# Performance work log

Measured on AMD Instinct MI355X. Metric: run time of the kernel, lower is better.

The kernel has to match this reference:

```python
import jax, jax.numpy as jnp
import numpy as np
import math

B, CK, CV, O, T, H, W = 2, 64, 512, 2, 16, 30, 54


def setup_inputs() -> dict:
    key = jax.random.key(0)
    k1, k2, k3, k4, k5 = jax.random.split(key, 5)
    return {
        'query_key': jax.random.normal(k1, (B, CK, H, W), jnp.float32),
        'query_selection': jax.random.uniform(k2, (B, CK, H, W), jnp.float32),
        'memory_key': jax.random.normal(k3, (B, CK, T, H, W), jnp.float32),
        'memory_shrinkage': jax.random.uniform(k4, (B, 1, T, H, W), jnp.float32),
        'memory_value': jax.random.normal(k5, (B, O, CV, T, H, W), jnp.float32),
    }


def reference(query_key, query_selection, memory_key, memory_shrinkage, memory_value):
    b, ck, h, w = query_key.shape
    t = memory_key.shape[2]
    n = t * h * w          # memory bank size
    hw = h * w             # query size
    o, cv = memory_value.shape[1], memory_value.shape[2]

    mk = memory_key.reshape(b, ck, n)             # B CK N
    ms = memory_shrinkage.reshape(b, 1, n)        # B 1 N
    qk = query_key.reshape(b, ck, hw)             # B CK HW
    qe = query_selection.reshape(b, ck, hw)       # B CK HW

    # negative squared L2 distance, selection-weighted per channel:
    # -sum_c qe_c * (mk_c - qk_c)^2 = -a_sq + 2ab - b_sq
    a_sq = jnp.einsum('bcn,bcq->bnq', mk * mk, qe)          # B N HW
    two_ab = 2.0 * jnp.einsum('bcn,bcq->bnq', mk, qk * qe)  # B N HW
    b_sq = jnp.sum(qe * qk * qk, axis=1, keepdims=True)     # B 1 HW
    similarity = (-a_sq + two_ab - b_sq)
    # shrinkage scaling + 1/sqrt(CK)
    similarity = similarity * ms.reshape(b, n, 1) * (1.0 / math.sqrt(ck))

    # softmax over the memory axis N
    affinity = jax.nn.softmax(similarity, axis=1)           # B N HW

    # weighted readout
    mv = memory_value.reshape(b, o * cv, n)                 # B (O*CV) N
    mem = jnp.einsum('bvn,bnq->bvq', mv, affinity)          # B (O*CV) HW
    return mem.reshape(b, o, cv, h, w)
```

## Files before the change

### kernel.cpp

```cpp
#include <hip/hip_runtime.h>
#include <stdint.h>

#define CK 64
#define CKP 128
#define OCV 1024
#define NTOT 25920
#define HW 1620
#define HWP 1664
#define QT 128
#define VT 256
#define NC 64
#define NQT 13
#define NVT 4
#define NSPLIT 2
#define CHUNKS_TOTAL 405
#define CHUNK_SPLIT 203

typedef _Float16 f16x8 __attribute__((ext_vector_type(8)));
typedef _Float16 f16x4 __attribute__((ext_vector_type(4)));
typedef float f32x4 __attribute__((ext_vector_type(4)));

__device__ __forceinline__ void gload_lds16(const void* g, void* l) {
  __builtin_amdgcn_global_load_lds(
      (const __attribute__((address_space(1))) uint32_t*)g,
      (__attribute__((address_space(3))) uint32_t*)l, 16, 0, 0);
}

__global__ void k_prep_mv(const float* __restrict__ mv, _Float16* __restrict__ mvh) {
  int i = blockIdx.x * 256 + threadIdx.x;
  const float4* s = (const float4*)mv + (size_t)i * 2;
  float4 a = s[0], b = s[1];
  f16x8 o;
  o[0]=(_Float16)a.x; o[1]=(_Float16)a.y; o[2]=(_Float16)a.z; o[3]=(_Float16)a.w;
  o[4]=(_Float16)b.x; o[5]=(_Float16)b.y; o[6]=(_Float16)b.z; o[7]=(_Float16)b.w;
  *((f16x8*)mvh + i) = o;
}

__global__ void k_prep_mk(const float* __restrict__ mk, _Float16* __restrict__ mkp) {
  __shared__ _Float16 LT[64 * CKP];
  int b = blockIdx.y, n0 = blockIdx.x * 64;
  int c4 = threadIdx.x >> 6, nl = threadIdx.x & 63;
  for (int c = c4; c < 64; c += 4) {
    float v = mk[((size_t)(b * 64 + c)) * NTOT + n0 + nl];
    LT[nl * CKP + c]      = (_Float16)v;
    LT[nl * CKP + 64 + c] = (_Float16)(v * v);
  }
  __syncthreads();
  #pragma unroll
  for (int k = 0; k < 4; ++k) {
    int idx = threadIdx.x + 256 * k;
    int n = idx >> 4, c16 = idx & 15;
    *((uint4*)(mkp + ((size_t)b * NTOT + n0 + n) * CKP + c16 * 8)) =
        *((const uint4*)(&LT[n * CKP + c16 * 8]));
  }
}

__global__ void k_prep_q(const float* __restrict__ qk, const float* __restrict__ qe,
                         _Float16* __restrict__ qp, float* __restrict__ bsq) {
  __shared__ _Float16 LT[QT * CKP];
  int b = blockIdx.y, q0 = blockIdx.x * QT;
  int t = threadIdx.x;
  int q = q0 + t;
  bool valid = q < HW;
  float acc = 0.f;
  for (int c = 0; c < 64; ++c) {
    float a = valid ? qk[((size_t)(b * 64 + c)) * HW + q] : 0.f;
    float e = valid ? qe[((size_t)(b * 64 + c)) * HW + q] : 0.f;
    LT[t * CKP + c]      = (_Float16)(2.f * a * e);
    LT[t * CKP + 64 + c] = (_Float16)(-e);
    acc += e * a * a;
  }
  bsq[(size_t)b * HWP + q] = acc;
  __syncthreads();
  #pragma unroll
  for (int k = 0; k < 16; ++k) {
    int idx = t + 128 * k;
    int qq = idx >> 4, c16 = idx & 15;
    *((uint4*)(qp + ((size_t)b * HWP + q0 + qq) * CKP + c16 * 8)) =
        *((const uint4*)(&LT[qq * CKP + c16 * 8]));
  }
}

__launch_bounds__(512, 1)
__global__ void k_main(const _Float16* __restrict__ mvh, const _Float16* __restrict__ mkp,
                       const _Float16* __restrict__ qp, const float* __restrict__ bsq,
                       const float* __restrict__ ms,
                       float* __restrict__ pO, float* __restrict__ lpart) {
  const int qt = blockIdx.x, vt = blockIdx.y;
  const int b = blockIdx.z >> 1, nsp = blockIdx.z & 1;
  const int tid = threadIdx.x;
  const int w = tid >> 6, l = tid & 63;
  const int l15 = l & 15, g = l >> 4;

  __shared__ _Float16 Qs[QT * CKP];
  __shared__ _Float16 MKs[2][NC * CKP];
  __shared__ _Float16 MVs[2][VT * NC];
  __shared__ _Float16 Ps[QT * NC];
  __shared__ float bsqs[QT];
  __shared__ float lred[QT * 8];

  const int qw = w & 3, nh = w >> 2;
  const int wv = w & 3, wq = w >> 2;

  const int cBeg = nsp ? CHUNK_SPLIT : 0;
  const int cEnd = nsp ? CHUNKS_TOTAL : CHUNK_SPLIT;

  const char* mvb[4]; int dmv[4];
  #pragma unroll
  for (int k = 0; k < 4; ++k) {
    int idx = k * 512 + tid;
    int v = idx >> 3, s = idx & 7, j = s ^ (v & 7);
    mvb[k] = (const char*)(mvh + ((size_t)b * OCV + vt * VT + v) * NTOT + j * 8);
    dmv[k] = idx * 16;
  }
  const char* mkb[2]; int dmk[2];
  #pragma unroll
  for (int k = 0; k < 2; ++k) {
    int idx = k * 512 + tid;
    int n = idx >> 4, s = idx & 15, j = s ^ (n & 7);
    mkb[k] = (const char*)(mkp + ((size_t)b * NTOT + n) * CKP + j * 8);
    dmk[k] = idx * 16;
  }
  const float* msb = ms + (size_t)b * NTOT + nh * 32 + g * 4;

  {
    size_t omv = (size_t)cBeg * (NC * 2);
    size_t omk = (size_t)cBeg * (NC * CKP * 2);
    #pragma unroll
    for (int k = 0; k < 4; ++k) gload_lds16(mvb[k] + omv, (char*)MVs[0] + dmv[k]);
    #pragma unroll
    for (int k = 0; k < 2; ++k) gload_lds16(mkb[k] + omk, (char*)MKs[0] + dmk[k]);
  }
  #pragma unroll
  for (int k = 0; k < 4; ++k) {
    int s = tid + k * 512;
    int q = s >> 4, kb = s & 15;
    uint4 v = *((const uint4*)(qp + ((size_t)b * HWP + qt * QT + q) * CKP + kb * 8));
    *((uint4*)(&Qs[q * CKP + ((kb ^ (q & 7)) * 8)])) = v;
  }
  if (tid < QT) bsqs[tid] = bsq[(size_t)b * HWP + qt * QT + tid];
  __syncthreads();

  f32x4 acc[4][4];
  #pragma unroll
  for (int i = 0; i < 4; ++i)
    #pragma unroll
    for (int j = 0; j < 4; ++j) acc[i][j] = (f32x4)0.f;
  float lp0 = 0.f, lp1 = 0.f;

  int cur = 0;
  for (int ch = cBeg; ch < cEnd; ++ch) {
    const float4 msA = *(const float4*)(msb + (size_t)ch * NC);
    const float4 msB = *(const float4*)(msb + (size_t)ch * NC + 16);
    __builtin_amdgcn_sched_barrier(0);
    if (ch + 1 < cEnd) {
      size_t omv = (size_t)(ch + 1) * (NC * 2);
      size_t omk = (size_t)(ch + 1) * (NC * CKP * 2);
      char* dv = (char*)MVs[cur ^ 1];
      char* dk = (char*)MKs[cur ^ 1];
      #pragma unroll
      for (int k = 0; k < 4; ++k) gload_lds16(mvb[k] + omv, dv + dmv[k]);
      #pragma unroll
      for (int k = 0; k < 2; ++k) gload_lds16(mkb[k] + omk, dk + dmk[k]);
    }

    const _Float16* MKc = MKs[cur];
    f32x4 sacc[2][2];
    #pragma unroll
    for (int i = 0; i < 2; ++i)
      #pragma unroll
      for (int j = 0; j < 2; ++j) sacc[i][j] = (f32x4)0.f;
    #pragma unroll
    for (int ks = 0; ks < 4; ++ks) {
      f16x8 af[2], bf[2];
      #pragma unroll
      for (int i = 0; i < 2; ++i) {
        int n_loc = nh * 32 + i * 16 + l15;
        af[i] = *((const f16x8*)(&MKc[n_loc * CKP + (((ks * 4 + g) ^ (n_loc & 7)) * 8)]));
      }
      #pragma unroll
      for (int j = 0; j < 2; ++j) {
        int q_loc = qw * 32 + j * 16 + l15;
        bf[j] = *((const f16x8*)(&Qs[q_loc * CKP + (((ks * 4 + g) ^ (q_loc & 7)) * 8)]));
      }
      #pragma unroll
      for (int i = 0; i < 2; ++i)
        #pragma unroll
        for (int j = 0; j < 2; ++j)
          sacc[i][j] = __builtin_amdgcn_mfma_f32_16x16x32_f16(af[i], bf[j], sacc[i][j], 0, 0, 0);
    }

    const float K = 0.125f * 1.44269504f;
    #pragma unroll
    for (int i = 0; i < 2; ++i) {
      int nbase = nh * 32 + i * 16 + g * 4;
      float m0 = (i ? msB.x : msA.x) * K;
      float m1 = (i ? msB.y : msA.y) * K;
      float m2 = (i ? msB.z : msA.z) * K;
      float m3 = (i ? msB.w : msA.w) * K;
      #pragma unroll
      for (int j = 0; j < 2; ++j) {
        int q_loc = qw * 32 + j * 16 + l15;
        float bqv = bsqs[q_loc];
        float p0 = exp2f((sacc[i][j][0] - bqv) * m0);
        float p1 = exp2f((sacc[i][j][1] - bqv) * m1);
        float p2 = exp2f((sacc[i][j][2] - bqv) * m2);
        float p3 = exp2f((sacc[i][j][3] - bqv) * m3);
        float psum = (p0 + p1) + (p2 + p3);
        if (j == 0) lp0 += psum; else lp1 += psum;
        f16x4 ph;
        ph[0]=(_Float16)p0; ph[1]=(_Float16)p1; ph[2]=(_Float16)p2; ph[3]=(_Float16)p3;
        int nb = nbase >> 3;
        int off4 = nbase & 7;
        *((f16x4*)(&Ps[q_loc * NC + ((nb ^ (q_loc & 7)) * 8) + off4])) = ph;
      }
    }

    asm volatile("s_waitcnt lgkmcnt(0)" ::: "memory");
    __builtin_amdgcn_s_barrier();
    __builtin_amdgcn_sched_barrier(0);

    const _Float16* MVc = MVs[cur];
    #pragma unroll
    for (int ks = 0; ks < 2; ++ks) {
      f16x8 av[4], bp[4];
      #pragma unroll
      for (int i = 0; i < 4; ++i) {
        int v_loc = wv * 64 + i * 16 + l15;
        av[i] = *((const f16x8*)(&MVc[v_loc * NC + (((ks * 4 + g) ^ (v_loc & 7)) * 8)]));
      }
      #pragma unroll
      for (int j = 0; j < 4; ++j) {
        int q_loc = wq * 64 + j * 16 + l15;
        bp[j] = *((const f16x8*)(&Ps[q_loc * NC + (((ks * 4 + g) ^ (q_loc & 7)) * 8)]));
      }
      #pragma unroll
      for (int i = 0; i < 4; ++i)
        #pragma unroll
        for (int j = 0; j < 4; ++j)
          acc[i][j] = __builtin_amdgcn_mfma_f32_16x16x32_f16(av[i], bp[j], acc[i][j], 0, 0, 0);
    }

    asm volatile("s_waitcnt vmcnt(0)" ::: "memory");
    __builtin_amdgcn_s_barrier();
    __builtin_amdgcn_sched_barrier(0);
    cur ^= 1;
  }

  {
    int q0a = qw * 32 + l15;
    lred[q0a * 8 + nh * 4 + g] = lp0;
    lred[(q0a + 16) * 8 + nh * 4 + g] = lp1;
  }
  __syncthreads();
  if (tid < QT) {
    float s = 0.f;
    #pragma unroll
    for (int j = 0; j < 8; ++j) s += lred[tid * 8 + j];
    lpart[((size_t)b * NSPLIT + nsp) * HWP + qt * QT + tid] = s;
  }
  #pragma unroll
  for (int i = 0; i < 4; ++i) {
    #pragma unroll
    for (int j = 0; j < 4; ++j) {
      #pragma unroll
      for (int r = 0; r < 4; ++r) {
        int v_glob = vt * VT + wv * 64 + i * 16 + g * 4 + r;
        int q_l = qt * QT + wq * 64 + j * 16 + l15;
        pO[(((size_t)b * NSPLIT + nsp) * OCV + v_glob) * HWP + q_l] = acc[i][j][r];
      }
    }
  }
}

__global__ void k_reduce(const float* __restrict__ pO, const float* __restrict__ lpart,
                         float* __restrict__ out) {
  int i = blockIdx.x * 256 + threadIdx.x;
  int q4 = i % 405;
  int rest = i / 405;
  int v = rest & (OCV - 1);
  int b = rest >> 10;
  int q = q4 * 4;
  const float4 p0 = *((const float4*)(pO + (((size_t)b * NSPLIT + 0) * OCV + v) * HWP + q));
  const float4 p1 = *((const float4*)(pO + (((size_t)b * NSPLIT + 1) * OCV + v) * HWP + q));
  const float4 l0 = *((const float4*)(lpart + ((size_t)b * NSPLIT + 0) * HWP + q));
  const float4 l1 = *((const float4*)(lpart + ((size_t)b * NSPLIT + 1) * HWP + q));
  float4 o;
  o.x = (p0.x + p1.x) / (l0.x + l1.x);
  o.y = (p0.y + p1.y) / (l0.y + l1.y);
  o.z = (p0.z + p1.z) / (l0.z + l1.z);
  o.w = (p0.w + p1.w) / (l0.w + l1.w);
  *((float4*)(out + ((size_t)b * OCV + v) * HW + q)) = o;
}

extern "C" void kernel_launch(void* const* d_in, const int* in_sizes, int n_in,
                              void* d_out, int out_size, void* d_ws, size_t ws_size,
                              hipStream_t stream) {
  const float* qk = (const float*)d_in[0];
  const float* qe = (const float*)d_in[1];
  const float* mk = (const float*)d_in[2];
  const float* ms = (const float*)d_in[3];
  const float* mv = (const float*)d_in[4];
  float* out = (float*)d_out;

  char* p = (char*)d_ws;
  _Float16* mvh = (_Float16*)p; p += (size_t)2 * OCV * NTOT * 2;
  _Float16* mkp = (_Float16*)p; p += (size_t)2 * NTOT * CKP * 2;
  _Float16* qp  = (_Float16*)p; p += (size_t)2 * HWP * CKP * 2;
  float* bsqw   = (float*)p;    p += (size_t)2 * HWP * 4;
  float* lpart  = (float*)p;    p += (size_t)2 * NSPLIT * HWP * 4;
  float* pO     = (float*)p;    p += (size_t)2 * NSPLIT * OCV * HWP * 4;
  size_t need = (size_t)(p - (char*)d_ws);
  if (ws_size < need) return;

  k_prep_mv<<<25920, 256, 0, stream>>>(mv, mvh);
  k_prep_mk<<<dim3(405, 2), 256, 0, stream>>>(mk, mkp);
  k_prep_q<<<dim3(NQT, 2), QT, 0, stream>>>(qk, qe, qp, bsqw);
  k_main<<<dim3(NQT, NVT, 4), 512, 0, stream>>>(mvh, mkp, qp, bsqw, ms, pO, lpart);
  k_reduce<<<3240, 256, 0, stream>>>(pO, lpart, out);
}
```

Before: 552.3 us.

## Software-pipeline score and readout stages, keep Q in registers, widen N-split

```diff
diff --git a/kernel.cpp b/kernel.cpp
--- a/kernel.cpp
+++ b/kernel.cpp
@@ -1,7 +1,6 @@
 #include <hip/hip_runtime.h>
 #include <stdint.h>
 
-#define CK 64
 #define CKP 128
 #define OCV 1024
 #define NTOT 25920
@@ -12,9 +11,7 @@
 #define NC 64
 #define NQT 13
 #define NVT 4
-#define NSPLIT 2
 #define CHUNKS_TOTAL 405
-#define CHUNK_SPLIT 203
 
 typedef _Float16 f16x8 __attribute__((ext_vector_type(8)));
 typedef _Float16 f16x4 __attribute__((ext_vector_type(4)));
@@ -85,25 +82,25 @@
 __global__ void k_main(const _Float16* __restrict__ mvh, const _Float16* __restrict__ mkp,
                        const _Float16* __restrict__ qp, const float* __restrict__ bsq,
                        const float* __restrict__ ms,
-                       float* __restrict__ pO, float* __restrict__ lpart) {
+                       float* __restrict__ pO, float* __restrict__ lpart,
+                       int NS, int CPN) {
   const int qt = blockIdx.x, vt = blockIdx.y;
-  const int b = blockIdx.z >> 1, nsp = blockIdx.z & 1;
+  const int b = blockIdx.z & 1, nsp = blockIdx.z >> 1;
   const int tid = threadIdx.x;
   const int w = tid >> 6, l = tid & 63;
   const int l15 = l & 15, g = l >> 4;
 
-  __shared__ _Float16 Qs[QT * CKP];
+  __shared__ _Float16 MVs[2][VT * NC];
   __shared__ _Float16 MKs[2][NC * CKP];
-  __shared__ _Float16 MVs[2][VT * NC];
-  __shared__ _Float16 Ps[QT * NC];
-  __shared__ float bsqs[QT];
+  __shared__ _Float16 Ps[2][QT * NC];
   __shared__ float lred[QT * 8];
 
   const int qw = w & 3, nh = w >> 2;
   const int wv = w & 3, wq = w >> 2;
 
-  const int cBeg = nsp ? CHUNK_SPLIT : 0;
-  const int cEnd = nsp ? CHUNKS_TOTAL : CHUNK_SPLIT;
+  const int cBeg = nsp * CPN;
+  int ce = cBeg + CPN; if (ce > CHUNKS_TOTAL) ce = CHUNKS_TOTAL;
+  const int cEnd = ce;
 
   const char* mvb[4]; int dmv[4];
   #pragma unroll
@@ -123,23 +120,16 @@
   }
   const float* msb = ms + (size_t)b * NTOT + nh * 32 + g * 4;
 
-  {
-    size_t omv = (size_t)cBeg * (NC * 2);
-    size_t omk = (size_t)cBeg * (NC * CKP * 2);
-    #pragma unroll
-    for (int k = 0; k < 4; ++k) gload_lds16(mvb[k] + omv, (char*)MVs[0] + dmv[k]);
-    #pragma unroll
-    for (int k = 0; k < 2; ++k) gload_lds16(mkb[k] + omk, (char*)MKs[0] + dmk[k]);
-  }
-  #pragma unroll
-  for (int k = 0; k < 4; ++k) {
-    int s = tid + k * 512;
-    int q = s >> 4, kb = s & 15;
-    uint4 v = *((const uint4*)(qp + ((size_t)b * HWP + qt * QT + q) * CKP + kb * 8));
-    *((uint4*)(&Qs[q * CKP + ((kb ^ (q & 7)) * 8)])) = v;
-  }
-  if (tid < QT) bsqs[tid] = bsq[(size_t)b * HWP + qt * QT + tid];
-  __syncthreads();
+  f16x8 qreg[2][4];
+  float bq[2];
+  #pragma unroll
+  for (int j = 0; j < 2; ++j) {
+    int q_loc = qw * 32 + j * 16 + l15;
+    const _Float16* qrow = qp + ((size_t)b * HWP + qt * QT + q_loc) * CKP;
+    #pragma unroll
+    for (int ks = 0; ks < 4; ++ks) qreg[j][ks] = *((const f16x8*)(qrow + (ks * 4 + g) * 8));
+    bq[j] = bsq[(size_t)b * HWP + qt * QT + q_loc];
+  }
 
   f32x4 acc[4][4];
   #pragma unroll
@@ -148,79 +138,70 @@
     for (int j = 0; j < 4; ++j) acc[i][j] = (f32x4)0.f;
   float lp0 = 0.f, lp1 = 0.f;
 
-  int cur = 0;
-  for (int ch = cBeg; ch < cEnd; ++ch) {
-    const float4 msA = *(const float4*)(msb + (size_t)ch * NC);
-    const float4 msB = *(const float4*)(msb + (size_t)ch * NC + 16);
-    __builtin_amdgcn_sched_barrier(0);
-    if (ch + 1 < cEnd) {
-      size_t omv = (size_t)(ch + 1) * (NC * 2);
-      size_t omk = (size_t)(ch + 1) * (NC * CKP * 2);
-      char* dv = (char*)MVs[cur ^ 1];
-      char* dk = (char*)MKs[cur ^ 1];
-      #pragma unroll
-      for (int k = 0; k < 4; ++k) gload_lds16(mvb[k] + omv, dv + dmv[k]);
-      #pragma unroll
-      for (int k = 0; k < 2; ++k) gload_lds16(mkb[k] + omk, dk + dmk[k]);
-    }
-
-    const _Float16* MKc = MKs[cur];
+  auto stage_mv = [&](int ch, int buf) {
+    size_t o = (size_t)ch * (NC * 2);
+    char* d = (char*)MVs[buf];
+    #pragma unroll
+    for (int k = 0; k < 4; ++k) gload_lds16(mvb[k] + o, d + dmv[k]);
+  };
+  auto stage_mk = [&](int ch, int buf) {
+    size_t o = (size_t)ch * (NC * CKP * 2);
+    char* d = (char*)MKs[buf];
+    #pragma unroll
+    for (int k = 0; k < 2; ++k) gload_lds16(mkb[k] + o, d + dmk[k]);
+  };
+
+  auto do_S = [&](int kb, int pb, float4 mA, float4 mB) {
+    const _Float16* MKc = MKs[kb];
     f32x4 sacc[2][2];
     #pragma unroll
-    for (int i = 0; i < 2; ++i)
-      #pragma unroll
-      for (int j = 0; j < 2; ++j) sacc[i][j] = (f32x4)0.f;
+    for (int i2 = 0; i2 < 2; ++i2)
+      #pragma unroll
+      for (int j = 0; j < 2; ++j) sacc[i2][j] = (f32x4)0.f;
     #pragma unroll
     for (int ks = 0; ks < 4; ++ks) {
-      f16x8 af[2], bf[2];
-      #pragma unroll
-      for (int i = 0; i < 2; ++i) {
-        int n_loc = nh * 32 + i * 16 + l15;
-        af[i] = *((const f16x8*)(&MKc[n_loc * CKP + (((ks * 4 + g) ^ (n_loc & 7)) * 8)]));
-      }
+      f16x8 af[2];
+      #pragma unroll
+      for (int i2 = 0; i2 < 2; ++i2) {
+        int n_loc = nh * 32 + i2 * 16 + l15;
+        af[i2] = *((const f16x8*)(&MKc[n_loc * CKP + (((ks * 4 + g) ^ (n_loc & 7)) * 8)]));
+      }
+      #pragma unroll
+      for (int i2 = 0; i2 < 2; ++i2)
+        #pragma unroll
+        for (int j = 0; j < 2; ++j)
+          sacc[i2][j] = __builtin_amdgcn_mfma_f32_16x16x32_f16(af[i2], qreg[j][ks], sacc[i2][j], 0, 0, 0);
+    }
+    const float K = 0.125f * 1.44269504f;
+    #pragma unroll
+    for (int i2 = 0; i2 < 2; ++i2) {
+      int nbase = nh * 32 + i2 * 16 + g * 4;
+      float m0 = (i2 ? mB.x : mA.x) * K;
+      float m1 = (i2 ? mB.y : mA.y) * K;
+      float m2 = (i2 ? mB.z : mA.z) * K;
+      float m3 = (i2 ? mB.w : mA.w) * K;
       #pragma unroll
       for (int j = 0; j < 2; ++j) {
         int q_loc = qw * 32 + j * 16 + l15;
-        bf[j] = *((const f16x8*)(&Qs[q_loc * CKP + (((ks * 4 + g) ^ (q_loc & 7)) * 8)]));
-      }
-      #pragma unroll
-      for (int i = 0; i < 2; ++i)
-        #pragma unroll
-        for (int j = 0; j < 2; ++j)
-          sacc[i][j] = __builtin_amdgcn_mfma_f32_16x16x32_f16(af[i], bf[j], sacc[i][j], 0, 0, 0);
-    }
-
-    const float K = 0.125f * 1.44269504f;
-    #pragma unroll
-    for (int i = 0; i < 2; ++i) {
-      int nbase = nh * 32 + i * 16 + g * 4;
-      float m0 = (i ? msB.x : msA.x) * K;
-      float m1 = (i ? msB.y : msA.y) * K;
-      float m2 = (i ? msB.z : msA.z) * K;
-      float m3 = (i ? msB.w : msA.w) * K;
-      #pragma unroll
-      for (int j = 0; j < 2; ++j) {
-        int q_loc = qw * 32 + j * 16 + l15;
-        float bqv = bsqs[q_loc];
-        float p0 = exp2f((sacc[i][j][0] - bqv) * m0);
-        float p1 = exp2f((sacc[i][j][1] - bqv) * m1);
-        float p2 = exp2f((sacc[i][j][2] - bqv) * m2);
-        float p3 = exp2f((sacc[i][j][3] - bqv) * m3);
+        float bqv = bq[j];
+        float p0 = exp2f((sacc[i2][j][0] - bqv) * m0);
+        float p1 = exp2f((sacc[i2][j][1] - bqv) * m1);
+        float p2 = exp2f((sacc[i2][j][2] - bqv) * m2);
+        float p3 = exp2f((sacc[i2][j][3] - bqv) * m3);
         float psum = (p0 + p1) + (p2 + p3);
         if (j == 0) lp0 += psum; else lp1 += psum;
         f16x4 ph;
         ph[0]=(_Float16)p0; ph[1]=(_Float16)p1; ph[2]=(_Float16)p2; ph[3]=(_Float16)p3;
         int nb = nbase >> 3;
         int off4 = nbase & 7;
-        *((f16x4*)(&Ps[q_loc * NC + ((nb ^ (q_loc & 7)) * 8) + off4])) = ph;
-      }
-    }
-
-    asm volatile("s_waitcnt lgkmcnt(0)" ::: "memory");
-    __builtin_amdgcn_s_barrier();
-    __builtin_amdgcn_sched_barrier(0);
-
-    const _Float16* MVc = MVs[cur];
+        *((f16x4*)(&Ps[pb][q_loc * NC + ((nb ^ (q_loc & 7)) * 8) + off4])) = ph;
+      }
+    }
+  };
+
+  auto do_RO = [&](int mb, int pb) {
+    const _Float16* MVc = MVs[mb];
+    const _Float16* Pc = Ps[pb];
     #pragma unroll
     for (int ks = 0; ks < 2; ++ks) {
       f16x8 av[4], bp[4];
@@ -232,7 +213,7 @@
       #pragma unroll
       for (int j = 0; j < 4; ++j) {
         int q_loc = wq * 64 + j * 16 + l15;
-        bp[j] = *((const f16x8*)(&Ps[q_loc * NC + (((ks * 4 + g) ^ (q_loc & 7)) * 8)]));
+        bp[j] = *((const f16x8*)(&Pc[q_loc * NC + (((ks * 4 + g) ^ (q_loc & 7)) * 8)]));
       }
       #pragma unroll
       for (int i = 0; i < 4; ++i)
@@ -240,11 +221,39 @@
         for (int j = 0; j < 4; ++j)
           acc[i][j] = __builtin_amdgcn_mfma_f32_16x16x32_f16(av[i], bp[j], acc[i][j], 0, 0, 0);
     }
-
-    asm volatile("s_waitcnt vmcnt(0)" ::: "memory");
+  };
+
+  stage_mv(cBeg, 0);
+  stage_mk(cBeg, 0);
+  if (cBeg + 1 < cEnd) stage_mk(cBeg + 1, 1);
+  float4 mA0 = *(const float4*)(msb + (size_t)cBeg * NC);
+  float4 mB0 = *(const float4*)(msb + (size_t)cBeg * NC + 16);
+  asm volatile("s_waitcnt vmcnt(0)" ::: "memory");
+  __builtin_amdgcn_s_barrier();
+  __builtin_amdgcn_sched_barrier(0);
+  do_S(0, 0, mA0, mB0);
+  asm volatile("s_waitcnt lgkmcnt(0)" ::: "memory");
+  __builtin_amdgcn_s_barrier();
+  __builtin_amdgcn_sched_barrier(0);
+
+  const int numCh = cEnd - cBeg;
+  for (int i = 0; i < numCh; ++i) {
+    const int ch = cBeg + i;
+    const int cur = i & 1, nxt = cur ^ 1;
+    const bool hv = (ch + 1 < cEnd);
+    float4 mA, mB;
+    if (hv) {
+      mA = *(const float4*)(msb + (size_t)(ch + 1) * NC);
+      mB = *(const float4*)(msb + (size_t)(ch + 1) * NC + 16);
+    }
+    __builtin_amdgcn_sched_barrier(0);
+    if (hv) stage_mv(ch + 1, nxt);
+    if (ch + 2 < cEnd) stage_mk(ch + 2, cur);
+    if (hv) do_S(nxt, nxt, mA, mB);
+    do_RO(cur, cur);
+    asm volatile("s_waitcnt vmcnt(0) lgkmcnt(0)" ::: "memory");
     __builtin_amdgcn_s_barrier();
     __builtin_amdgcn_sched_barrier(0);
-    cur ^= 1;
   }
 
   {
@@ -257,7 +266,7 @@
     float s = 0.f;
     #pragma unroll
     for (int j = 0; j < 8; ++j) s += lred[tid * 8 + j];
-    lpart[((size_t)b * NSPLIT + nsp) * HWP + qt * QT + tid] = s;
+    lpart[((size_t)(b * NS + nsp)) * HWP + qt * QT + tid] = s;
   }
   #pragma unroll
   for (int i = 0; i < 4; ++i) {
@@ -267,29 +276,30 @@
       for (int r = 0; r < 4; ++r) {
         int v_glob = vt * VT + wv * 64 + i * 16 + g * 4 + r;
         int q_l = qt * QT + wq * 64 + j * 16 + l15;
-        pO[(((size_t)b * NSPLIT + nsp) * OCV + v_glob) * HWP + q_l] = acc[i][j][r];
+        pO[(((size_t)(b * NS + nsp)) * OCV + v_glob) * HWP + q_l] = acc[i][j][r];
       }
     }
   }
 }
 
 __global__ void k_reduce(const float* __restrict__ pO, const float* __restrict__ lpart,
-                         float* __restrict__ out) {
+                         float* __restrict__ out, int NS) {
   int i = blockIdx.x * 256 + threadIdx.x;
   int q4 = i % 405;
   int rest = i / 405;
   int v = rest & (OCV - 1);
   int b = rest >> 10;
   int q = q4 * 4;
-  const float4 p0 = *((const float4*)(pO + (((size_t)b * NSPLIT + 0) * OCV + v) * HWP + q));
-  const float4 p1 = *((const float4*)(pO + (((size_t)b * NSPLIT + 1) * OCV + v) * HWP + q));
-  const float4 l0 = *((const float4*)(lpart + ((size_t)b * NSPLIT + 0) * HWP + q));
-  const float4 l1 = *((const float4*)(lpart + ((size_t)b * NSPLIT + 1) * HWP + q));
+  float apx = 0.f, apy = 0.f, apz = 0.f, apw = 0.f;
+  float alx = 0.f, aly = 0.f, alz = 0.f, alw = 0.f;
+  for (int s = 0; s < NS; ++s) {
+    const float4 p = *((const float4*)(pO + (((size_t)(b * NS + s)) * OCV + v) * HWP + q));
+    const float4 lv = *((const float4*)(lpart + ((size_t)(b * NS + s)) * HWP + q));
+    apx += p.x; apy += p.y; apz += p.z; apw += p.w;
+    alx += lv.x; aly += lv.y; alz += lv.z; alw += lv.w;
+  }
   float4 o;
-  o.x = (p0.x + p1.x) / (l0.x + l1.x);
-  o.y = (p0.y + p1.y) / (l0.y + l1.y);
-  o.z = (p0.z + p1.z) / (l0.z + l1.z);
-  o.w = (p0.w + p1.w) / (l0.w + l1.w);
+  o.x = apx / alx; o.y = apy / aly; o.z = apz / alz; o.w = apw / alw;
   *((float4*)(out + ((size_t)b * OCV + v) * HW + q)) = o;
 }
 
@@ -303,19 +313,29 @@
   const float* mv = (const float*)d_in[4];
   float* out = (float*)d_out;
 
+  const size_t sz_mvh = (size_t)2 * OCV * NTOT * 2;
+  const size_t sz_mkp = (size_t)2 * NTOT * CKP * 2;
+  const size_t sz_qp  = (size_t)2 * HWP * CKP * 2;
+  const size_t sz_bsq = (size_t)2 * HWP * 4;
+  const size_t base   = sz_mvh + sz_mkp + sz_qp + sz_bsq;
+  auto need = [&](int ns) {
+    return base + (size_t)2 * ns * HWP * 4 + (size_t)2 * ns * OCV * HWP * 4;
+  };
+  int NS = (ws_size >= need(4)) ? 4 : 2;
+  if (ws_size < need(NS)) return;
+  const int CPN = (CHUNKS_TOTAL + NS - 1) / NS;
+
   char* p = (char*)d_ws;
-  _Float16* mvh = (_Float16*)p; p += (size_t)2 * OCV * NTOT * 2;
-  _Float16* mkp = (_Float16*)p; p += (size_t)2 * NTOT * CKP * 2;
-  _Float16* qp  = (_Float16*)p; p += (size_t)2 * HWP * CKP * 2;
-  float* bsqw   = (float*)p;    p += (size_t)2 * HWP * 4;
-  float* lpart  = (float*)p;    p += (size_t)2 * NSPLIT * HWP * 4;
-  float* pO     = (float*)p;    p += (size_t)2 * NSPLIT * OCV * HWP * 4;
-  size_t need = (size_t)(p - (char*)d_ws);
-  if (ws_size < need) return;
+  _Float16* mvh = (_Float16*)p; p += sz_mvh;
+  _Float16* mkp = (_Float16*)p; p += sz_mkp;
+  _Float16* qp  = (_Float16*)p; p += sz_qp;
+  float* bsqw   = (float*)p;    p += sz_bsq;
+  float* lpart  = (float*)p;    p += (size_t)2 * NS * HWP * 4;
+  float* pO     = (float*)p;
 
   k_prep_mv<<<25920, 256, 0, stream>>>(mv, mvh);
   k_prep_mk<<<dim3(405, 2), 256, 0, stream>>>(mk, mkp);
   k_prep_q<<<dim3(NQT, 2), QT, 0, stream>>>(qk, qe, qp, bsqw);
-  k_main<<<dim3(NQT, NVT, 4), 512, 0, stream>>>(mvh, mkp, qp, bsqw, ms, pO, lpart);
-  k_reduce<<<3240, 256, 0, stream>>>(pO, lpart, out);
-}
+  k_main<<<dim3(NQT, NVT, 2 * NS), 512, 0, stream>>>(mvh, mkp, qp, bsqw, ms, pO, lpart, NS, CPN);
+  k_reduce<<<3240, 256, 0, stream>>>(pO, lpart, out, NS);
+}
```

Measured after the change: 580.1 us. 5.0% more time.
